# Kernel optimization log

Measured on AMD Instinct MI355X. Metric: run time of the kernel, lower is better.

The kernel has to match this reference:

```python
import jax, jax.numpy as jnp
import numpy as np

B, T, D = 32, 512, 1024
P, E, K = 512, 256, 14
NH, L, FF, TOPK = 4, 2, 2048, 7
FOLD_DIV = 2
EPS = 1e-5


def _ln(x, g, b):
    m = x.mean(-1, keepdims=True)
    v = ((x - m) ** 2).mean(-1, keepdims=True)
    return (x - m) * jax.lax.rsqrt(v + EPS) * g + b


def _bn(x, g, b, m, v):  # eval-mode BatchNorm1d with running stats
    return (x - m) * jax.lax.rsqrt(v + EPS) * g + b


def _attn(q, k, v, nh):
    Bq, Tq, Eq = q.shape
    Tk = k.shape[1]
    hd = Eq // nh
    qh = q.reshape(Bq, Tq, nh, hd).transpose(0, 2, 1, 3)
    kh = k.reshape(Bq, Tk, nh, hd).transpose(0, 2, 1, 3)
    vh = v.reshape(Bq, Tk, nh, hd).transpose(0, 2, 1, 3)
    s = jnp.einsum('bhqd,bhkd->bhqk', qh, kh) / jnp.sqrt(jnp.float32(hd))
    a = jax.nn.softmax(s, axis=-1)
    o = jnp.einsum('bhqk,bhkd->bhqd', a, vh)
    return o.transpose(0, 2, 1, 3).reshape(Bq, Tq, Eq)


def setup_inputs() -> dict:
    key = jax.random.key(0)
    ks = iter(jax.random.split(key, 64))

    def rn(shape, s=0.02):
        return jax.random.normal(next(ks), shape, jnp.float32) * s

    return dict(
        x=jax.random.normal(next(ks), (B, T, D), jnp.float32),
        pred_w=rn((D,)), pred_b=jnp.zeros(()),
        t_wqkv=rn((L, D, 3 * D)), t_bqkv=jnp.zeros((L, 3 * D)),
        t_wo=rn((L, D, D)), t_bo=jnp.zeros((L, D)),
        t_ln1g=jnp.ones((L, D)), t_ln1b=jnp.zeros((L, D)),
        t_w1=rn((L, D, FF)), t_b1=jnp.zeros((L, FF)),
        t_w2=rn((L, FF, D)), t_b2=jnp.zeros((L, D)),
        t_ln2g=jnp.ones((L, D)), t_ln2b=jnp.zeros((L, D)),
        sb_w=rn((D, P)), sb_b=jnp.zeros((P,)),
        bn1_g=jnp.ones((P,)), bn1_b=jnp.zeros((P,)), bn1_m=jnp.zeros((P,)), bn1_v=jnp.ones((P,)),
        dt_w=rn((P,)), dt_b=jnp.zeros(()),
        cc_w1=rn((P, 256)), cc_b1=jnp.zeros((256,)),
        bn2_g=jnp.ones((256,)), bn2_b=jnp.zeros((256,)), bn2_m=jnp.zeros((256,)), bn2_v=jnp.ones((256,)),
        cc_w2=rn((256, K)), cc_b2=jnp.zeros((K,)),
        ce=rn((K, E), 1.0),
        kp_w=rn((P, E)), kp_b=jnp.zeros((E,)),
        ca_wqkv=rn((E, 3 * E)), ca_bqkv=jnp.zeros((3 * E,)),
        ca_wo=rn((E, E)), ca_bo=jnp.zeros((E,)),
        fp_w=rn((E, D)), fp_b=jnp.zeros((D,)),
        df_w=rn((P,)), df_b=jnp.zeros(()),
    )


def reference(x, pred_w, pred_b, t_wqkv, t_bqkv, t_wo, t_bo, t_ln1g, t_ln1b, t_w1, t_b1,
              t_w2, t_b2, t_ln2g, t_ln2b, sb_w, sb_b, bn1_g, bn1_b, bn1_m, bn1_v,
              dt_w, dt_b, cc_w1, cc_b1, bn2_g, bn2_b, bn2_m, bn2_v, cc_w2, cc_b2,
              ce, kp_w, kp_b, ca_wqkv, ca_bqkv, ca_wo, ca_bo, fp_w, fp_b, df_w, df_b):
    # --- GlobalAdaptiveTSM: per-token adaptive channel shift, fully vectorized ---
    ratio = jax.nn.sigmoid(jnp.einsum('btd,d->bt', x, pred_w) + pred_b)  # ShiftPredictor
    fold = D // FOLD_DIV
    sn = (ratio * fold).astype(jnp.int32)[..., None]                     # [B,T,1]
    z = jnp.zeros_like(x[:, :1])
    x_prev = jnp.concatenate([z, x[:, :-1]], axis=1)   # t=0 region stays zero
    x_next = jnp.concatenate([x[:, 1:], z], axis=1)    # t=T-1 region stays zero
    c = jnp.arange(D)
    h = jnp.where(c < sn, x_prev, jnp.where(c < 2 * sn, x_next, x))
    # --- TemporalTransformer: 2 post-norm encoder layers (eval mode) ---
    for l in range(L):
        qkv = h @ t_wqkv[l] + t_bqkv[l]
        q, k, v = jnp.split(qkv, 3, axis=-1)
        a = _attn(q, k, v, NH) @ t_wo[l] + t_bo[l]
        h = _ln(h + a, t_ln1g[l], t_ln1b[l])
        f = jax.nn.relu(h @ t_w1[l] + t_b1[l]) @ t_w2[l] + t_b2[l]
        h = _ln(h + f, t_ln2g[l], t_ln2b[l])

    def backbone(zz):
        return jax.nn.relu(_bn(zz @ sb_w + sb_b, bn1_g, bn1_b, bn1_m, bn1_v))

    shared = backbone(h)                                      # [B,T,P]
    top_scores = jnp.einsum('btp,p->bt', shared, dt_w) + dt_b
    _, idx = jax.lax.top_k(top_scores, TOPK)
    agg = jnp.take_along_axis(shared, idx[..., None], axis=1).mean(1)  # [B,P]
    c1 = jax.nn.relu(_bn(agg @ cc_w1 + cc_b1, bn2_g, bn2_b, bn2_m, bn2_v))
    logits = c1 @ cc_w2 + cc_b2                               # [B,K]
    cat_emb = jax.nn.softmax(logits, axis=-1) @ ce            # [B,E]
    proj = shared @ kp_w + kp_b                               # [B,T,E]
    q = cat_emb[:, None, :] @ ca_wqkv[:, :E] + ca_bqkv[:E]
    k = proj @ ca_wqkv[:, E:2 * E] + ca_bqkv[E:2 * E]
    v = proj @ ca_wqkv[:, 2 * E:] + ca_bqkv[2 * E:]
    ctx = _attn(q, k, v, NH) @ ca_wo + ca_bo                  # [B,1,E] broadcasts over T
    final = proj + ctx
    fin_proj = backbone(final @ fp_w + fp_b)
    seg = jnp.einsum('btp,p->bt', fin_proj, df_w) + df_b
    return seg, logits
```

## Files before the change

### kernel.cpp

```cpp
#include <hip/hip_runtime.h>
#include <math.h>

#define Bz 32
#define Tz 512
#define Dz 1024
#define Pz 512
#define Ez 256
#define KC 14
#define NHz 4
#define Lz 2
#define FFz 2048
#define TOPKz 7
#define EPSz 1e-5f
#define BT (Bz*Tz)

typedef unsigned short ushort_t;
typedef __attribute__((ext_vector_type(8))) short short8;
typedef __attribute__((ext_vector_type(4))) float f32x4;

__device__ __forceinline__ ushort_t f2bf(float f) {
    union { float f; unsigned int u; } x; x.f = f;
    unsigned int r = x.u + 0x7fffu + ((x.u >> 16) & 1u);
    return (ushort_t)(r >> 16);
}
__device__ __forceinline__ float bf2f(ushort_t h) {
    union { unsigned int u; float f; } x; x.u = ((unsigned int)h) << 16; return x.f;
}

__global__ __launch_bounds__(256) void mgemm_k(
    const ushort_t* __restrict__ A, int lda,
    const ushort_t* __restrict__ Wt,
    const float* __restrict__ bias,
    float* __restrict__ Cf, ushort_t* __restrict__ Ch, int ldc,
    int Kd, int epi,
    const float* __restrict__ bng, const float* __restrict__ bnb,
    const float* __restrict__ bnm, const float* __restrict__ bnv)
{
    __shared__ __align__(16) ushort_t As[128 * 32];
    __shared__ __align__(16) ushort_t Bs[128 * 32];
    const int tid = threadIdx.x;
    const int lane = tid & 63, wid = tid >> 6;
    const int row0 = blockIdx.y * 128, col0 = blockIdx.x * 128;
    const int wrow = (wid >> 1) * 64, wcol = (wid & 1) * 64;
    const int srow = (lane >> 2);
    const int skoff = (lane & 3) * 8;

    f32x4 acc[4][4];
    const f32x4 zr = {0.f, 0.f, 0.f, 0.f};
    #pragma unroll
    for (int m = 0; m < 4; m++)
        #pragma unroll
        for (int n = 0; n < 4; n++) acc[m][n] = zr;

    for (int k0 = 0; k0 < Kd; k0 += 32) {
        #pragma unroll
        for (int j = 0; j < 2; j++) {
            const int r = wid * 32 + j * 16;
            const ushort_t* ga = A + (size_t)(row0 + r + srow) * lda + k0 + skoff;
            __builtin_amdgcn_global_load_lds(
                (const __attribute__((address_space(1))) unsigned int*)ga,
                (__attribute__((address_space(3))) unsigned int*)(As + r * 32), 16, 0, 0);
            const ushort_t* gb = Wt + (size_t)(col0 + r + srow) * Kd + k0 + skoff;
            __builtin_amdgcn_global_load_lds(
                (const __attribute__((address_space(1))) unsigned int*)gb,
                (__attribute__((address_space(3))) unsigned int*)(Bs + r * 32), 16, 0, 0);
        }
        __syncthreads();
        short8 af[4], bf[4];
        #pragma unroll
        for (int m = 0; m < 4; m++)
            af[m] = *(const short8*)(As + (wrow + m * 16 + (lane & 15)) * 32 + (lane >> 4) * 8);
        #pragma unroll
        for (int n = 0; n < 4; n++)
            bf[n] = *(const short8*)(Bs + (wcol + n * 16 + (lane & 15)) * 32 + (lane >> 4) * 8);
        #pragma unroll
        for (int m = 0; m < 4; m++)
            #pragma unroll
            for (int n = 0; n < 4; n++)
                acc[m][n] = __builtin_amdgcn_mfma_f32_16x16x32_bf16(af[m], bf[n], acc[m][n], 0, 0, 0);
        __syncthreads();
    }

    #pragma unroll
    for (int n = 0; n < 4; n++) {
        const int ccol = col0 + wcol + n * 16 + (lane & 15);
        const float bb = bias[ccol];
        float bsc = 1.f, bsh = 0.f;
        if (epi == 2) {
            bsc = rsqrtf(bnv[ccol] + EPSz) * bng[ccol];
            bsh = bnb[ccol] - bnm[ccol] * bsc;
        }
        #pragma unroll
        for (int m = 0; m < 4; m++) {
            #pragma unroll
            for (int r = 0; r < 4; r++) {
                const int crow = row0 + wrow + m * 16 + (lane >> 4) * 4 + r;
                float y = acc[m][n][r] + bb;
                if (epi == 2) y = y * bsc + bsh;
                if (epi >= 1) y = fmaxf(y, 0.f);
                if (Cf) Cf[(size_t)crow * ldc + ccol] = y;
                if (Ch) Ch[(size_t)crow * ldc + ccol] = f2bf(y);
            }
        }
    }
}

__global__ __launch_bounds__(256) void bgemm_k(
    const ushort_t* __restrict__ A0, int lda, size_t Abz, int Ahz,
    const ushort_t* __restrict__ W0, int ldw, size_t Wbz, int Whz,
    float* __restrict__ Cf0, ushort_t* __restrict__ Ch0, int ldc, size_t Cbz, int Chz, int Kd)
{
    const int z = blockIdx.z, bl = z >> 2, hh = z & 3;
    const ushort_t* A = A0 + (size_t)bl * Abz + (size_t)hh * Ahz;
    const ushort_t* W = W0 + (size_t)bl * Wbz + (size_t)hh * Whz;

    __shared__ __align__(16) ushort_t As[128 * 32];
    __shared__ __align__(16) ushort_t Bs[128 * 32];
    const int tid = threadIdx.x;
    const int lane = tid & 63, wid = tid >> 6;
    const int row0 = blockIdx.y * 128, col0 = blockIdx.x * 128;
    const int wrow = (wid >> 1) * 64, wcol = (wid & 1) * 64;
    const int srow = (lane >> 2);
    const int skoff = (lane & 3) * 8;

    f32x4 acc[4][4];
    const f32x4 zr = {0.f, 0.f, 0.f, 0.f};
    #pragma unroll
    for (int m = 0; m < 4; m++)
        #pragma unroll
        for (int n = 0; n < 4; n++) acc[m][n] = zr;

    for (int k0 = 0; k0 < Kd; k0 += 32) {
        #pragma unroll
        for (int j = 0; j < 2; j++) {
            const int r = wid * 32 + j * 16;
            const ushort_t* ga = A + (size_t)(row0 + r + srow) * lda + k0 + skoff;
            __builtin_amdgcn_global_load_lds(
                (const __attribute__((address_space(1))) unsigned int*)ga,
                (__attribute__((address_space(3))) unsigned int*)(As + r * 32), 16, 0, 0);
            const ushort_t* gb = W + (size_t)(col0 + r + srow) * ldw + k0 + skoff;
            __builtin_amdgcn_global_load_lds(
                (const __attribute__((address_space(1))) unsigned int*)gb,
                (__attribute__((address_space(3))) unsigned int*)(Bs + r * 32), 16, 0, 0);
        }
        __syncthreads();
        short8 af[4], bf[4];
        #pragma unroll
        for (int m = 0; m < 4; m++)
            af[m] = *(const short8*)(As + (wrow + m * 16 + (lane & 15)) * 32 + (lane >> 4) * 8);
        #pragma unroll
        for (int n = 0; n < 4; n++)
            bf[n] = *(const short8*)(Bs + (wcol + n * 16 + (lane & 15)) * 32 + (lane >> 4) * 8);
        #pragma unroll
        for (int m = 0; m < 4; m++)
            #pragma unroll
            for (int n = 0; n < 4; n++)
                acc[m][n] = __builtin_amdgcn_mfma_f32_16x16x32_bf16(af[m], bf[n], acc[m][n], 0, 0, 0);
        __syncthreads();
    }

    #pragma unroll
    for (int n = 0; n < 4; n++) {
        const int ccol = col0 + wcol + n * 16 + (lane & 15);
        #pragma unroll
        for (int m = 0; m < 4; m++) {
            #pragma unroll
            for (int r = 0; r < 4; r++) {
                const int crow = row0 + wrow + m * 16 + (lane >> 4) * 4 + r;
                const float y = acc[m][n][r];
                if (Cf0) (Cf0 + (size_t)bl * Cbz + (size_t)hh * Chz)[(size_t)crow * ldc + ccol] = y;
                if (Ch0) (Ch0 + (size_t)bl * Cbz + (size_t)hh * Chz)[(size_t)crow * ldc + ccol] = f2bf(y);
            }
        }
    }
}

__global__ __launch_bounds__(256) void qkvt_k(
    const ushort_t* __restrict__ qkvb, ushort_t* __restrict__ Sb, ushort_t* __restrict__ Vt)
{
    __shared__ __align__(16) ushort_t smem[2][128 * 32];
    const int bx = blockIdx.x, z = blockIdx.y;
    const int bl = z >> 2, hh = z & 3;
    const int tid = threadIdx.x;

    if (bx < 16) {
        const ushort_t* A = qkvb + (size_t)bl * 512 * 3072 + hh * 256;
        const ushort_t* W = qkvb + (size_t)bl * 512 * 3072 + 1024 + hh * 256;
        ushort_t* C = Sb + (size_t)z * 512 * 512;
        ushort_t* As = smem[0];
        ushort_t* Bs = smem[1];
        const int lane = tid & 63, wid = tid >> 6;
        const int row0 = (bx >> 2) * 128, col0 = (bx & 3) * 128;
        const int wrow = (wid >> 1) * 64, wcol = (wid & 1) * 64;
        const int srow = (lane >> 2);
        const int skoff = (lane & 3) * 8;

        f32x4 acc[4][4];
        const f32x4 zr = {0.f, 0.f, 0.f, 0.f};
        #pragma unroll
        for (int m = 0; m < 4; m++)
            #pragma unroll
            for (int n = 0; n < 4; n++) acc[m][n] = zr;

        for (int k0 = 0; k0 < 256; k0 += 32) {
            #pragma unroll
            for (int j = 0; j < 2; j++) {
                const int r = wid * 32 + j * 16;
                const ushort_t* ga = A + (size_t)(row0 + r + srow) * 3072 + k0 + skoff;
                __builtin_amdgcn_global_load_lds(
                    (const __attribute__((address_space(1))) unsigned int*)ga,
                    (__attribute__((address_space(3))) unsigned int*)(As + r * 32), 16, 0, 0);
                const ushort_t* gb = W + (size_t)(col0 + r + srow) * 3072 + k0 + skoff;
                __builtin_amdgcn_global_load_lds(
                    (const __attribute__((address_space(1))) unsigned int*)gb,
                    (__attribute__((address_space(3))) unsigned int*)(Bs + r * 32), 16, 0, 0);
            }
            __syncthreads();
            short8 af[4], bf[4];
            #pragma unroll
            for (int m = 0; m < 4; m++)
                af[m] = *(const short8*)(As + (wrow + m * 16 + (lane & 15)) * 32 + (lane >> 4) * 8);
            #pragma unroll
            for (int n = 0; n < 4; n++)
                bf[n] = *(const short8*)(Bs + (wcol + n * 16 + (lane & 15)) * 32 + (lane >> 4) * 8);
            #pragma unroll
            for (int m = 0; m < 4; m++)
                #pragma unroll
                for (int n = 0; n < 4; n++)
                    acc[m][n] = __builtin_amdgcn_mfma_f32_16x16x32_bf16(af[m], bf[n], acc[m][n], 0, 0, 0);
            __syncthreads();
        }

        #pragma unroll
        for (int n = 0; n < 4; n++) {
            const int ccol = col0 + wcol + n * 16 + (lane & 15);
            #pragma unroll
            for (int m = 0; m < 4; m++) {
                #pragma unroll
                for (int r = 0; r < 4; r++) {
                    const int crow = row0 + wrow + m * 16 + (lane >> 4) * 4 + r;
                    C[(size_t)crow * 512 + ccol] = f2bf(acc[m][n][r]);
                }
            }
        }
    } else {
        const int local = bx - 16;
        const int gx = (local & 7) * 32;
        const int gy = (local >> 3) * 32;
        const ushort_t* src = qkvb + (size_t)bl * 512 * 3072 + 2048 + hh * 256;
        ushort_t* dst = Vt + (size_t)z * 256 * 512;
        ushort_t (*t)[33] = (ushort_t(*)[33])smem;
        const int tx = tid & 31, ty = tid >> 5;
        #pragma unroll
        for (int i = 0; i < 4; i++) {
            const int row = ty + i * 8;
            t[row][tx] = src[(size_t)(gy + row) * 3072 + gx + tx];
        }
        __syncthreads();
        #pragma unroll
        for (int i = 0; i < 4; i++) {
            const int nr = ty + i * 8;
            dst[(size_t)(gx + nr) * 512 + gy + tx] = t[tx][nr];
        }
    }
}

__global__ __launch_bounds__(256) void softmax_k(ushort_t* __restrict__ SP)
{
    const int row = blockIdx.x * 4 + (threadIdx.x >> 6);
    const int lane = threadIdx.x & 63;
    ushort_t* rp = SP + (size_t)row * 512 + lane * 8;
    union { ushort_t h[8]; uint4 u; } in;
    in.u = *(const uint4*)rp;
    float v[8];
    #pragma unroll
    for (int i = 0; i < 8; i++) v[i] = bf2f(in.h[i]) * 0.0625f;
    float m = v[0];
    #pragma unroll
    for (int i = 1; i < 8; i++) m = fmaxf(m, v[i]);
    #pragma unroll
    for (int off = 32; off > 0; off >>= 1) m = fmaxf(m, __shfl_xor(m, off));
    float s = 0.f;
    #pragma unroll
    for (int i = 0; i < 8; i++) { v[i] = expf(v[i] - m); s += v[i]; }
    #pragma unroll
    for (int off = 32; off > 0; off >>= 1) s += __shfl_xor(s, off);
    const float inv = 1.f / s;
    union { ushort_t h[8]; uint4 u; } pk;
    #pragma unroll
    for (int i = 0; i < 8; i++) pk.h[i] = f2bf(v[i] * inv);
    *(uint4*)rp = pk.u;
}

struct WtJobs {
    const float* src[13];
    ushort_t*    dst[13];
    int ld[13];
    int Kd[13];
    int nx[13];
    int base[14];
};

__global__ __launch_bounds__(256) void wtall_k(WtJobs J)
{
    const int bid = blockIdx.x;
    int j = 0;
    #pragma unroll
    for (int i = 0; i < 12; i++) if (bid >= J.base[i + 1]) j = i + 1;
    const int local = bid - J.base[j];
    const int bx = local % J.nx[j], by = local / J.nx[j];
    const float* src = J.src[j];
    ushort_t* dst = J.dst[j];
    const int ld = J.ld[j], Kd = J.Kd[j];

    __shared__ float t[32][33];
    const int tx = threadIdx.x & 31, ty = threadIdx.x >> 5;
    const int gx = bx * 32;
    const int gy = by * 32;
    #pragma unroll
    for (int i = 0; i < 4; i++) {
        const int row = ty + i * 8;
        t[row][tx] = src[(size_t)(gy + row) * ld + gx + tx];
    }
    __syncthreads();
    #pragma unroll
    for (int i = 0; i < 4; i++) {
        const int nr = ty + i * 8;
        dst[(size_t)(gx + nr) * Kd + gy + tx] = f2bf(t[tx][nr]);
    }
}

__global__ __launch_bounds__(256) void predshift_k(
    const float* __restrict__ x, const float* __restrict__ pred_w,
    const float* __restrict__ pred_b, ushort_t* __restrict__ hb)
{
    const int row = blockIdx.x, tid = threadIdx.x;
    const size_t base = (size_t)row * Dz;
    float s = 0.f;
    #pragma unroll
    for (int i = 0; i < 4; i++) {
        int c = tid + i * 256;
        s += x[base + c] * pred_w[c];
    }
    __shared__ float red[256];
    __shared__ int sns;
    red[tid] = s; __syncthreads();
    for (int off = 128; off > 0; off >>= 1) {
        if (tid < off) red[tid] += red[tid + off];
        __syncthreads();
    }
    if (tid == 0) {
        float sg = 1.f / (1.f + expf(-(red[0] + pred_b[0])));
        sns = (int)(sg * (float)(Dz / 2));
    }
    __syncthreads();
    const int sn = sns;
    const int t = row & (Tz - 1);
    #pragma unroll
    for (int i = 0; i < 4; i++) {
        const int c = tid + i * 256;
        const size_t idx = base + c;
        float v;
        if (c < sn)          v = (t > 0)      ? x[idx - Dz] : 0.f;
        else if (c < 2 * sn) v = (t < Tz - 1) ? x[idx + Dz] : 0.f;
        else                 v = x[idx];
        hb[idx] = f2bf(v);
    }
}

__global__ __launch_bounds__(256) void addlnb_k(
    ushort_t* __restrict__ hb, const ushort_t* __restrict__ r,
    const float* __restrict__ g, const float* __restrict__ b)
{
    const int row = blockIdx.x, tid = threadIdx.x;
    const size_t base = (size_t)row * Dz;
    float x[4]; float s = 0.f, sq = 0.f;
    #pragma unroll
    for (int i = 0; i < 4; i++) {
        const int c = tid + i * 256;
        x[i] = bf2f(hb[base + c]) + bf2f(r[base + c]);
        s += x[i]; sq += x[i] * x[i];
    }
    __shared__ float rs[256], rq[256];
    rs[tid] = s; rq[tid] = sq; __syncthreads();
    for (int off = 128; off > 0; off >>= 1) {
        if (tid < off) { rs[tid] += rs[tid + off]; rq[tid] += rq[tid + off]; }
        __syncthreads();
    }
    float mean = rs[0] * (1.f / Dz);
    float var = rq[0] * (1.f / Dz) - mean * mean;
    float inv = rsqrtf(var + EPSz);
    #pragma unroll
    for (int i = 0; i < 4; i++) {
        int c = tid + i * 256;
        float y = (x[i] - mean) * inv * g[c] + b[c];
        hb[base + c] = f2bf(y);
    }
}

__global__ __launch_bounds__(256) void rowdot_k(
    const float* __restrict__ in, const float* __restrict__ w,
    const float* __restrict__ bptr, float* __restrict__ outf)
{
    const int row = blockIdx.x, tid = threadIdx.x;
    const float* r = in + (size_t)row * Pz;
    float s = 0.f;
    #pragma unroll
    for (int c = tid; c < Pz; c += 256) s += r[c] * w[c];
    __shared__ float red[256];
    red[tid] = s; __syncthreads();
    for (int off = 128; off > 0; off >>= 1) {
        if (tid < off) red[tid] += red[tid + off];
        __syncthreads();
    }
    if (tid == 0) outf[row] = red[0] + bptr[0];
}

__global__ __launch_bounds__(256) void tailcls_k(
    const float* __restrict__ scores, const float* __restrict__ shared_,
    const float* __restrict__ cc_w1, const float* __restrict__ cc_b1,
    const float* __restrict__ g2, const float* __restrict__ b2,
    const float* __restrict__ m2, const float* __restrict__ v2,
    const float* __restrict__ cc_w2, const float* __restrict__ cc_b2,
    const float* __restrict__ ce,
    const float* __restrict__ ca_wqkv, const float* __restrict__ ca_bqkv,
    float* __restrict__ logits_out, float* __restrict__ qx)
{
    const int b = blockIdx.x, tid = threadIdx.x;
    __shared__ float sv[Tz];
    __shared__ float rv[256]; __shared__ int ri[256];
    __shared__ int tki[TOPKz];
    __shared__ float ag[Pz], c1s[256], sm[16], cemb[256];

    sv[tid] = scores[b * Tz + tid];
    sv[tid + 256] = scores[b * Tz + tid + 256];
    __syncthreads();

    for (int it = 0; it < TOPKz; it++) {
        float v0 = sv[tid]; int i0 = tid;
        float v1 = sv[tid + 256];
        if (v1 > v0) { v0 = v1; i0 = tid + 256; }
        rv[tid] = v0; ri[tid] = i0; __syncthreads();
        for (int off = 128; off > 0; off >>= 1) {
            if (tid < off) {
                if (rv[tid + off] > rv[tid] ||
                    (rv[tid + off] == rv[tid] && ri[tid + off] < ri[tid])) {
                    rv[tid] = rv[tid + off]; ri[tid] = ri[tid + off];
                }
            }
            __syncthreads();
        }
        if (tid == 0) { tki[it] = ri[0]; sv[ri[0]] = -INFINITY; }
        __syncthreads();
    }

    const float* base = shared_ + (size_t)b * Tz * Pz;
    for (int p = tid; p < Pz; p += 256) {
        float s = 0.f;
        #pragma unroll
        for (int j = 0; j < TOPKz; j++) s += base[(size_t)tki[j] * Pz + p];
        ag[p] = s * (1.f / TOPKz);
    }
    __syncthreads();

    float s = 0.f;
    for (int p = 0; p < Pz; p++) s += ag[p] * cc_w1[p * 256 + tid];
    s += cc_b1[tid];
    s = (s - m2[tid]) * rsqrtf(v2[tid] + EPSz) * g2[tid] + b2[tid];
    s = fmaxf(s, 0.f);
    c1s[tid] = s;
    __syncthreads();
    if (tid < KC) {
        float l = 0.f;
        for (int e = 0; e < 256; e++) l += c1s[e] * cc_w2[e * KC + tid];
        l += cc_b2[tid];
        sm[tid] = l;
        logits_out[b * KC + tid] = l;
    }
    __syncthreads();
    if (tid == 0) {
        float mx = sm[0];
        for (int k = 1; k < KC; k++) mx = fmaxf(mx, sm[k]);
        float su = 0.f;
        for (int k = 0; k < KC; k++) { sm[k] = expf(sm[k] - mx); su += sm[k]; }
        float inv = 1.f / su;
        for (int k = 0; k < KC; k++) sm[k] *= inv;
    }
    __syncthreads();
    float cesum = 0.f;
    #pragma unroll
    for (int k = 0; k < KC; k++) cesum += sm[k] * ce[k * 256 + tid];
    cemb[tid] = cesum; __syncthreads();
    float q = 0.f;
    for (int i = 0; i < 256; i++) q += cemb[i] * ca_wqkv[i * 768 + tid];
    qx[b * 256 + tid] = q + ca_bqkv[tid];
}

__global__ __launch_bounds__(256) void xattn_k(
    const float* __restrict__ qx, const float* __restrict__ kv,
    const float* __restrict__ ca_wo, const float* __restrict__ ca_bo,
    float* __restrict__ ctx2)
{
    const int b = blockIdx.x, tid = threadIdx.x;
    __shared__ float q4[256];
    __shared__ float sc[NHz][Tz];
    __shared__ float cx[256];
    q4[tid] = qx[b * 256 + tid];
    __syncthreads();
    for (int si = tid; si < NHz * Tz; si += 256) {
        int hh = si >> 9, t = si & (Tz - 1);
        const float* kr = kv + ((size_t)b * Tz + t) * 512 + hh * 64;
        const float* qr = q4 + hh * 64;
        float s = 0.f;
        #pragma unroll 8
        for (int d = 0; d < 64; d++) s += qr[d] * kr[d];
        sc[hh][t] = s * 0.125f;
    }
    __syncthreads();
    const int hh = tid >> 6, lane = tid & 63;
    float mx = -INFINITY;
    for (int t = lane; t < Tz; t += 64) mx = fmaxf(mx, sc[hh][t]);
    for (int off = 32; off > 0; off >>= 1) mx = fmaxf(mx, __shfl_xor(mx, off));
    float su = 0.f;
    for (int t = lane; t < Tz; t += 64) { float e = expf(sc[hh][t] - mx); sc[hh][t] = e; su += e; }
    for (int off = 32; off > 0; off >>= 1) su += __shfl_xor(su, off);
    float inv = 1.f / su;
    __syncthreads();
    float acc = 0.f;
    for (int t = 0; t < Tz; t++) acc += sc[hh][t] * kv[((size_t)b * Tz + t) * 512 + 256 + tid];
    cx[tid] = acc * inv;
    __syncthreads();
    float s2 = 0.f;
    for (int i = 0; i < 256; i++) s2 += cx[i] * ca_wo[i * 256 + tid];
    ctx2[b * 256 + tid] = s2 + ca_bo[tid];
}

__global__ __launch_bounds__(256) void addctx_k(
    const float* __restrict__ proj, const float* __restrict__ ctx2, ushort_t* __restrict__ fb)
{
    size_t idx = (size_t)blockIdx.x * 256 + threadIdx.x;
    int e = (int)(idx & 255);
    int b = (int)(idx >> 17);
    fb[idx] = f2bf(proj[idx] + ctx2[b * 256 + e]);
}

extern "C" void kernel_launch(void* const* d_in, const int* in_sizes, int n_in,
                              void* d_out, int out_size, void* d_ws, size_t ws_size,
                              hipStream_t stream)
{
    const float* x       = (const float*)d_in[0];
    const float* pred_w  = (const float*)d_in[1];
    const float* pred_b  = (const float*)d_in[2];
    const float* t_wqkv  = (const float*)d_in[3];
    const float* t_bqkv  = (const float*)d_in[4];
    const float* t_wo    = (const float*)d_in[5];
    const float* t_bo    = (const float*)d_in[6];
    const float* t_ln1g  = (const float*)d_in[7];
    const float* t_ln1b  = (const float*)d_in[8];
    const float* t_w1    = (const float*)d_in[9];
    const float* t_b1    = (const float*)d_in[10];
    const float* t_w2    = (const float*)d_in[11];
    const float* t_b2    = (const float*)d_in[12];
    const float* t_ln2g  = (const float*)d_in[13];
    const float* t_ln2b  = (const float*)d_in[14];
    const float* sb_w    = (const float*)d_in[15];
    const float* sb_b    = (const float*)d_in[16];
    const float* bn1_g   = (const float*)d_in[17];
    const float* bn1_b   = (const float*)d_in[18];
    const float* bn1_m   = (const float*)d_in[19];
    const float* bn1_v   = (const float*)d_in[20];
    const float* dt_w    = (const float*)d_in[21];
    const float* dt_b    = (const float*)d_in[22];
    const float* cc_w1   = (const float*)d_in[23];
    const float* cc_b1   = (const float*)d_in[24];
    const float* bn2_g   = (const float*)d_in[25];
    const float* bn2_b   = (const float*)d_in[26];
    const float* bn2_m   = (const float*)d_in[27];
    const float* bn2_v   = (const float*)d_in[28];
    const float* cc_w2   = (const float*)d_in[29];
    const float* cc_b2   = (const float*)d_in[30];
    const float* ce      = (const float*)d_in[31];
    const float* kp_w    = (const float*)d_in[32];
    const float* kp_b    = (const float*)d_in[33];
    const float* ca_wqkv = (const float*)d_in[34];
    const float* ca_bqkv = (const float*)d_in[35];
    const float* ca_wo   = (const float*)d_in[36];
    const float* ca_bo   = (const float*)d_in[37];
    const float* fp_w    = (const float*)d_in[38];
    const float* fp_b    = (const float*)d_in[39];
    const float* df_w    = (const float*)d_in[40];
    const float* df_b    = (const float*)d_in[41];

    float* out = (float*)d_out;

    char* wp = (char*)d_ws;
    auto alloc = [&](size_t bytes) -> char* {
        char* r = wp; wp += (bytes + 255) & ~(size_t)255; return r;
    };
    float* scores  = (float*)alloc(BT * 4);
    float* qxbuf   = (float*)alloc((size_t)Bz * Ez * 4);
    float* ctx2buf = (float*)alloc((size_t)Bz * Ez * 4);

    const size_t WT_TOTAL = 2*(size_t)3072*1024 + 2*(size_t)1024*1024 + 2*(size_t)2048*1024
                          + 2*(size_t)1024*2048 + (size_t)512*1024 + (size_t)256*512
                          + 2*(size_t)256*256 + (size_t)1024*256;
    ushort_t* wtb = (ushort_t*)alloc(WT_TOTAL * 2);
    size_t woff = 0;
    auto nxt = [&](size_t n) -> ushort_t* { ushort_t* r = wtb + woff; woff += n; return r; };
    ushort_t* qkvT[2] = { nxt((size_t)3072*1024), nxt((size_t)3072*1024) };
    ushort_t* woT[2]  = { nxt((size_t)1024*1024), nxt((size_t)1024*1024) };
    ushort_t* w1T[2]  = { nxt((size_t)2048*1024), nxt((size_t)2048*1024) };
    ushort_t* w2T[2]  = { nxt((size_t)1024*2048), nxt((size_t)1024*2048) };
    ushort_t* sbT  = nxt((size_t)512*1024);
    ushort_t* kpT  = nxt((size_t)256*512);
    ushort_t* kvT  = nxt((size_t)512*256);
    ushort_t* fpT  = nxt((size_t)1024*256);

    size_t fixedB = (size_t)(wp - (char*)d_ws);
    int Bc = Bz;
    while (Bc > 1 && fixedB + (size_t)Bc * Tz * 14336 + 1048576 > ws_size) Bc >>= 1;
    const int Rmax = Bc * Tz;
    ushort_t* hb   = (ushort_t*)alloc((size_t)Rmax * 1024 * 2);
    ushort_t* qkvb = (ushort_t*)alloc((size_t)Rmax * 3072 * 2);
    ushort_t* Pb   = (ushort_t*)alloc((size_t)Rmax * 2048 * 2);
    ushort_t* Vt   = (ushort_t*)alloc((size_t)Rmax * 1024 * 2);

    {
        WtJobs J;
        const float* srcs[13] = { t_wqkv, t_wqkv + (size_t)1024*3072, t_wo, t_wo + (size_t)1024*1024,
                                  t_w1, t_w1 + (size_t)1024*2048, t_w2, t_w2 + (size_t)2048*1024,
                                  sb_w, kp_w, ca_wqkv + Ez, ca_wqkv + 2*Ez, fp_w };
        ushort_t* dsts[13] = { qkvT[0], qkvT[1], woT[0], woT[1], w1T[0], w1T[1], w2T[0], w2T[1],
                               sbT, kpT, kvT, kvT + (size_t)256*256, fpT };
        const int lds_[13] = { 3072, 3072, 1024, 1024, 2048, 2048, 1024, 1024, 512, 256, 768, 768, 1024 };
        const int kds_[13] = { 1024, 1024, 1024, 1024, 1024, 1024, 2048, 2048, 1024, 512, 256, 256, 256 };
        const int nxs_[13] = { 96, 96, 32, 32, 64, 64, 32, 32, 16, 8, 8, 8, 32 };
        const int nys_[13] = { 32, 32, 32, 32, 32, 32, 64, 64, 32, 16, 8, 8, 8 };
        int acc = 0;
        for (int i = 0; i < 13; i++) {
            J.src[i] = srcs[i]; J.dst[i] = dsts[i];
            J.ld[i] = lds_[i]; J.Kd[i] = kds_[i]; J.nx[i] = nxs_[i];
            J.base[i] = acc; acc += nxs_[i] * nys_[i];
        }
        J.base[13] = acc;
        wtall_k<<<acc, 256, 0, stream>>>(J);
    }

    for (int b0 = 0; b0 < Bz; b0 += Bc) {
        const int R = Bc * Tz;
        const float* xc = x + (size_t)b0 * Tz * Dz;

        auto MG = [&](const ushort_t* Ain, int lda, const ushort_t* Wt_, const float* bias,
                      float* Cf, ushort_t* Ch, int ldc, int N, int Kd, int epi,
                      const float* g = nullptr, const float* bb = nullptr,
                      const float* m = nullptr, const float* v = nullptr) {
            mgemm_k<<<dim3(N/128, R/128), 256, 0, stream>>>(
                Ain, lda, Wt_, bias, Cf, Ch, ldc, Kd, epi, g, bb, m, v);
        };

        predshift_k<<<R, 256, 0, stream>>>(xc, pred_w, pred_b, hb);

        for (int l = 0; l < Lz; l++) {
            MG(hb, 1024, qkvT[l], t_bqkv + (size_t)l*3072, nullptr, qkvb, 3072, 3072, 1024, 0);
            qkvt_k<<<dim3(144, Bc * 4), 256, 0, stream>>>(qkvb, Pb, Vt);
            softmax_k<<<R, 256, 0, stream>>>(Pb);
            bgemm_k<<<dim3(2, 4, Bc * 4), 256, 0, stream>>>(
                Pb, 512, (size_t)4 * 512 * 512, 512 * 512,
                Vt, 512, (size_t)4 * 256 * 512, 256 * 512,
                nullptr, qkvb, 3072, (size_t)512 * 3072, 256, 512);
            MG(qkvb, 3072, woT[l], t_bo + (size_t)l*1024, nullptr, Pb, 1024, 1024, 1024, 0);
            addlnb_k<<<R, 256, 0, stream>>>(hb, Pb,
                                            t_ln1g + (size_t)l*Dz, t_ln1b + (size_t)l*Dz);
            MG(hb, 1024, w1T[l], t_b1 + (size_t)l*FFz, nullptr, qkvb, 2048, 2048, 1024, 1);
            MG(qkvb, 2048, w2T[l], t_b2 + (size_t)l*Dz, nullptr, Pb, 1024, 1024, 2048, 0);
            addlnb_k<<<R, 256, 0, stream>>>(hb, Pb,
                                            t_ln2g + (size_t)l*Dz, t_ln2b + (size_t)l*Dz);
        }

        float*    shared  = (float*)Vt;
        float*    proj    = (float*)hb;
        float*    kvb     = (float*)(qkvb + (size_t)R * 1024);
        float*    fin     = (float*)(Pb + (size_t)R * 1024);
        ushort_t* sharedb = Pb;
        ushort_t* projb   = Pb + (size_t)R * 512;
        ushort_t* fb      = Pb + (size_t)R * 768;
        ushort_t* fpb     = qkvb;

        MG(hb, 1024, sbT, sb_b, shared, sharedb, 512, 512, 1024, 2, bn1_g, bn1_b, bn1_m, bn1_v);
        rowdot_k<<<R, 256, 0, stream>>>(shared, dt_w, dt_b, scores + (size_t)b0 * Tz);
        tailcls_k<<<Bc, 256, 0, stream>>>(scores + (size_t)b0 * Tz, shared, cc_w1, cc_b1,
                                          bn2_g, bn2_b, bn2_m, bn2_v, cc_w2, cc_b2,
                                          ce, ca_wqkv, ca_bqkv,
                                          out + BT + (size_t)b0 * KC, qxbuf);
        MG(sharedb, 512, kpT, kp_b, proj, projb, 256, 256, 512, 0);
        MG(projb, 256, kvT, ca_bqkv + Ez, kvb, nullptr, 512, 512, 256, 0);
        xattn_k<<<Bc, 256, 0, stream>>>(qxbuf, kvb, ca_wo, ca_bo, ctx2buf);
        addctx_k<<<(R * Ez) / 256, 256, 0, stream>>>(proj, ctx2buf, fb);
        MG(fb, 256, fpT, fp_b, nullptr, fpb, 1024, 1024, 256, 0);
        MG(fpb, 1024, sbT, sb_b, fin, nullptr, 512, 512, 1024, 2, bn1_g, bn1_b, bn1_m, bn1_v);
        rowdot_k<<<R, 256, 0, stream>>>(fin, df_w, df_b, out + (size_t)b0 * Tz);
    }
}
```

Before: 1.757 ms.

## Fuse attention QK^T, softmax and PV into one kernel with LDS-resident probabilities

Measured after the change: 1.520 ms. -13.5%, faster.

```diff
diff --git a/kernel.cpp b/kernel.cpp
--- a/kernel.cpp
+++ b/kernel.cpp
@@ -27,6 +27,10 @@
     union { unsigned int u; float f; } x; x.u = ((unsigned int)h) << 16; return x.f;
 }
 
+#define GLDS(gp, lp) __builtin_amdgcn_global_load_lds( \
+    (const __attribute__((address_space(1))) unsigned int*)(gp), \
+    (__attribute__((address_space(3))) unsigned int*)(lp), 16, 0, 0)
+
 __global__ __launch_bounds__(256) void mgemm_k(
     const ushort_t* __restrict__ A, int lda,
     const ushort_t* __restrict__ Wt,
@@ -56,14 +60,8 @@
         #pragma unroll
         for (int j = 0; j < 2; j++) {
             const int r = wid * 32 + j * 16;
-            const ushort_t* ga = A + (size_t)(row0 + r + srow) * lda + k0 + skoff;
-            __builtin_amdgcn_global_load_lds(
-                (const __attribute__((address_space(1))) unsigned int*)ga,
-                (__attribute__((address_space(3))) unsigned int*)(As + r * 32), 16, 0, 0);
-            const ushort_t* gb = Wt + (size_t)(col0 + r + srow) * Kd + k0 + skoff;
-            __builtin_amdgcn_global_load_lds(
-                (const __attribute__((address_space(1))) unsigned int*)gb,
-                (__attribute__((address_space(3))) unsigned int*)(Bs + r * 32), 16, 0, 0);
+            GLDS(A + (size_t)(row0 + r + srow) * lda + k0 + skoff, As + r * 32);
+            GLDS(Wt + (size_t)(col0 + r + srow) * Kd + k0 + skoff, Bs + r * 32);
         }
         __syncthreads();
         short8 af[4], bf[4];
@@ -105,191 +103,189 @@
     }
 }
 
-__global__ __launch_bounds__(256) void bgemm_k(
-    const ushort_t* __restrict__ A0, int lda, size_t Abz, int Ahz,
-    const ushort_t* __restrict__ W0, int ldw, size_t Wbz, int Whz,
-    float* __restrict__ Cf0, ushort_t* __restrict__ Ch0, int ldc, size_t Cbz, int Chz, int Kd)
+__global__ __launch_bounds__(1024) void flash_k(
+    ushort_t* __restrict__ qkvb, const ushort_t* __restrict__ Vt)
+{
+    __shared__ __align__(16) ushort_t Plds[128 * 512];
+    __shared__ __align__(16) ushort_t Bs2[256 * 32];
+    __shared__ float red[128][4];
+    ushort_t* As = Plds;
+    ushort_t* Bs = Plds + 128 * 32;
+
+    const int z = blockIdx.y, bl = z >> 2, hh = z & 3;
+    const int row0 = blockIdx.x * 128;
+    ushort_t* Qs = qkvb + (size_t)bl * 512 * 3072 + hh * 256;
+    const ushort_t* Ks = qkvb + (size_t)bl * 512 * 3072 + 1024 + hh * 256;
+    const ushort_t* V = Vt + (size_t)z * 256 * 512;
+    const int tid = threadIdx.x, lane = tid & 63, w = tid >> 6;
+    const int wr = w >> 2, wc = w & 3;
+
+    f32x4 acc[2][8];
+    const f32x4 zr = {0.f, 0.f, 0.f, 0.f};
+    #pragma unroll
+    for (int m = 0; m < 2; m++)
+        #pragma unroll
+        for (int n = 0; n < 8; n++) acc[m][n] = zr;
+
+    for (int d0 = 0; d0 < 256; d0 += 32) {
+        if (w < 8) {
+            const int rbu = w * 16;
+            const int row = rbu + (lane >> 2);
+            GLDS(Qs + (size_t)(row0 + row) * 3072 + d0 + (lane & 3) * 8, As + rbu * 32);
+        } else {
+            #pragma unroll
+            for (int i = 0; i < 4; i++) {
+                const int rbu = (w - 8) * 64 + i * 16;
+                const int row = rbu + (lane >> 2);
+                GLDS(Ks + (size_t)row * 3072 + d0 + (lane & 3) * 8, Bs + rbu * 32);
+            }
+        }
+        __syncthreads();
+        short8 af[2];
+        #pragma unroll
+        for (int m = 0; m < 2; m++)
+            af[m] = *(const short8*)(As + (wr * 32 + m * 16 + (lane & 15)) * 32 + (lane >> 4) * 8);
+        #pragma unroll
+        for (int n = 0; n < 8; n++) {
+            const short8 bfv = *(const short8*)(Bs + (wc * 128 + n * 16 + (lane & 15)) * 32 + (lane >> 4) * 8);
+            #pragma unroll
+            for (int m = 0; m < 2; m++)
+                acc[m][n] = __builtin_amdgcn_mfma_f32_16x16x32_bf16(af[m], bfv, acc[m][n], 0, 0, 0);
+        }
+        __syncthreads();
+    }
+
+    #pragma unroll
+    for (int m = 0; m < 2; m++)
+        #pragma unroll
+        for (int n = 0; n < 8; n++) acc[m][n] *= 0.0625f;
+
+    float rmx[2][4], rinv[2][4];
+    #pragma unroll
+    for (int m = 0; m < 2; m++)
+        #pragma unroll
+        for (int r = 0; r < 4; r++) {
+            float mx = acc[m][0][r];
+            #pragma unroll
+            for (int n = 1; n < 8; n++) mx = fmaxf(mx, acc[m][n][r]);
+            mx = fmaxf(mx, __shfl_xor(mx, 1));
+            mx = fmaxf(mx, __shfl_xor(mx, 2));
+            mx = fmaxf(mx, __shfl_xor(mx, 4));
+            mx = fmaxf(mx, __shfl_xor(mx, 8));
+            if ((lane & 15) == 0) red[wr * 32 + m * 16 + (lane >> 4) * 4 + r][wc] = mx;
+        }
+    __syncthreads();
+    #pragma unroll
+    for (int m = 0; m < 2; m++)
+        #pragma unroll
+        for (int r = 0; r < 4; r++) {
+            const int rw = wr * 32 + m * 16 + (lane >> 4) * 4 + r;
+            rmx[m][r] = fmaxf(fmaxf(red[rw][0], red[rw][1]), fmaxf(red[rw][2], red[rw][3]));
+        }
+    __syncthreads();
+    #pragma unroll
+    for (int m = 0; m < 2; m++)
+        #pragma unroll
+        for (int r = 0; r < 4; r++) {
+            float s = 0.f;
+            #pragma unroll
+            for (int n = 0; n < 8; n++) {
+                const float e = expf(acc[m][n][r] - rmx[m][r]);
+                acc[m][n][r] = e; s += e;
+            }
+            s += __shfl_xor(s, 1); s += __shfl_xor(s, 2);
+            s += __shfl_xor(s, 4); s += __shfl_xor(s, 8);
+            if ((lane & 15) == 0) red[wr * 32 + m * 16 + (lane >> 4) * 4 + r][wc] = s;
+        }
+    __syncthreads();
+    #pragma unroll
+    for (int m = 0; m < 2; m++)
+        #pragma unroll
+        for (int r = 0; r < 4; r++) {
+            const int rw = wr * 32 + m * 16 + (lane >> 4) * 4 + r;
+            rinv[m][r] = 1.f / (red[rw][0] + red[rw][1] + red[rw][2] + red[rw][3]);
+        }
+    __syncthreads();
+
+    char* Pc = (char*)Plds;
+    #pragma unroll
+    for (int m = 0; m < 2; m++)
+        #pragma unroll
+        for (int r = 0; r < 4; r++) {
+            const int rw = wr * 32 + m * 16 + (lane >> 4) * 4 + r;
+            const int rx = (rw & 7) << 4;
+            #pragma unroll
+            for (int n = 0; n < 8; n++) {
+                const int col = wc * 128 + n * 16 + (lane & 15);
+                *(ushort_t*)(Pc + (((rw * 512 + col) * 2) ^ rx)) = f2bf(acc[m][n][r] * rinv[m][r]);
+            }
+        }
+    __syncthreads();
+
+    f32x4 acc2[2][4];
+    #pragma unroll
+    for (int m = 0; m < 2; m++)
+        #pragma unroll
+        for (int n = 0; n < 4; n++) acc2[m][n] = zr;
+
+    for (int k0 = 0; k0 < 512; k0 += 32) {
+        {
+            const int rbu = w * 16;
+            const int row = rbu + (lane >> 2);
+            GLDS(V + (size_t)row * 512 + k0 + (lane & 3) * 8, Bs2 + rbu * 32);
+        }
+        __syncthreads();
+        short8 af2[2];
+        #pragma unroll
+        for (int m = 0; m < 2; m++) {
+            const int rw = wr * 32 + m * 16 + (lane & 15);
+            const int rx = (rw & 7) << 4;
+            af2[m] = *(const short8*)(Pc + (((rw * 512 + k0 + (lane >> 4) * 8) * 2) ^ rx));
+        }
+        #pragma unroll
+        for (int n = 0; n < 4; n++) {
+            const short8 bfv = *(const short8*)(Bs2 + (wc * 64 + n * 16 + (lane & 15)) * 32 + (lane >> 4) * 8);
+            #pragma unroll
+            for (int m = 0; m < 2; m++)
+                acc2[m][n] = __builtin_amdgcn_mfma_f32_16x16x32_bf16(af2[m], bfv, acc2[m][n], 0, 0, 0);
+        }
+        __syncthreads();
+    }
+
+    #pragma unroll
+    for (int n = 0; n < 4; n++) {
+        const int ccol = wc * 64 + n * 16 + (lane & 15);
+        #pragma unroll
+        for (int m = 0; m < 2; m++)
+            #pragma unroll
+            for (int r = 0; r < 4; r++) {
+                const int crow = row0 + wr * 32 + m * 16 + (lane >> 4) * 4 + r;
+                Qs[(size_t)crow * 3072 + ccol] = f2bf(acc2[m][n][r]);
+            }
+    }
+}
+
+__global__ __launch_bounds__(256) void vtb_k(
+    const ushort_t* __restrict__ qkvb, ushort_t* __restrict__ Vt)
 {
     const int z = blockIdx.z, bl = z >> 2, hh = z & 3;
-    const ushort_t* A = A0 + (size_t)bl * Abz + (size_t)hh * Ahz;
-    const ushort_t* W = W0 + (size_t)bl * Wbz + (size_t)hh * Whz;
-
-    __shared__ __align__(16) ushort_t As[128 * 32];
-    __shared__ __align__(16) ushort_t Bs[128 * 32];
-    const int tid = threadIdx.x;
-    const int lane = tid & 63, wid = tid >> 6;
-    const int row0 = blockIdx.y * 128, col0 = blockIdx.x * 128;
-    const int wrow = (wid >> 1) * 64, wcol = (wid & 1) * 64;
-    const int srow = (lane >> 2);
-    const int skoff = (lane & 3) * 8;
-
-    f32x4 acc[4][4];
-    const f32x4 zr = {0.f, 0.f, 0.f, 0.f};
-    #pragma unroll
-    for (int m = 0; m < 4; m++)
-        #pragma unroll
-        for (int n = 0; n < 4; n++) acc[m][n] = zr;
-
-    for (int k0 = 0; k0 < Kd; k0 += 32) {
-        #pragma unroll
-        for (int j = 0; j < 2; j++) {
-            const int r = wid * 32 + j * 16;
-            const ushort_t* ga = A + (size_t)(row0 + r + srow) * lda + k0 + skoff;
-            __builtin_amdgcn_global_load_lds(
-                (const __attribute__((address_space(1))) unsigned int*)ga,
-                (__attribute__((address_space(3))) unsigned int*)(As + r * 32), 16, 0, 0);
-            const ushort_t* gb = W + (size_t)(col0 + r + srow) * ldw + k0 + skoff;
-            __builtin_amdgcn_global_load_lds(
-                (const __attribute__((address_space(1))) unsigned int*)gb,
-                (__attribute__((address_space(3))) unsigned int*)(Bs + r * 32), 16, 0, 0);
-        }
-        __syncthreads();
-        short8 af[4], bf[4];
-        #pragma unroll
-        for (int m = 0; m < 4; m++)
-            af[m] = *(const short8*)(As + (wrow + m * 16 + (lane & 15)) * 32 + (lane >> 4) * 8);
-        #pragma unroll
-        for (int n = 0; n < 4; n++)
-            bf[n] = *(const short8*)(Bs + (wcol + n * 16 + (lane & 15)) * 32 + (lane >> 4) * 8);
-        #pragma unroll
-        for (int m = 0; m < 4; m++)
-            #pragma unroll
-            for (int n = 0; n < 4; n++)
-                acc[m][n] = __builtin_amdgcn_mfma_f32_16x16x32_bf16(af[m], bf[n], acc[m][n], 0, 0, 0);
-        __syncthreads();
-    }
-
-    #pragma unroll
-    for (int n = 0; n < 4; n++) {
-        const int ccol = col0 + wcol + n * 16 + (lane & 15);
-        #pragma unroll
-        for (int m = 0; m < 4; m++) {
-            #pragma unroll
-            for (int r = 0; r < 4; r++) {
-                const int crow = row0 + wrow + m * 16 + (lane >> 4) * 4 + r;
-                const float y = acc[m][n][r];
-                if (Cf0) (Cf0 + (size_t)bl * Cbz + (size_t)hh * Chz)[(size_t)crow * ldc + ccol] = y;
-                if (Ch0) (Ch0 + (size_t)bl * Cbz + (size_t)hh * Chz)[(size_t)crow * ldc + ccol] = f2bf(y);
-            }
-        }
-    }
-}
-
-__global__ __launch_bounds__(256) void qkvt_k(
-    const ushort_t* __restrict__ qkvb, ushort_t* __restrict__ Sb, ushort_t* __restrict__ Vt)
-{
-    __shared__ __align__(16) ushort_t smem[2][128 * 32];
-    const int bx = blockIdx.x, z = blockIdx.y;
-    const int bl = z >> 2, hh = z & 3;
-    const int tid = threadIdx.x;
-
-    if (bx < 16) {
-        const ushort_t* A = qkvb + (size_t)bl * 512 * 3072 + hh * 256;
-        const ushort_t* W = qkvb + (size_t)bl * 512 * 3072 + 1024 + hh * 256;
-        ushort_t* C = Sb + (size_t)z * 512 * 512;
-        ushort_t* As = smem[0];
-        ushort_t* Bs = smem[1];
-        const int lane = tid & 63, wid = tid >> 6;
-        const int row0 = (bx >> 2) * 128, col0 = (bx & 3) * 128;
-        const int wrow = (wid >> 1) * 64, wcol = (wid & 1) * 64;
-        const int srow = (lane >> 2);
-        const int skoff = (lane & 3) * 8;
-
-        f32x4 acc[4][4];
-        const f32x4 zr = {0.f, 0.f, 0.f, 0.f};
-        #pragma unroll
-        for (int m = 0; m < 4; m++)
-            #pragma unroll
-            for (int n = 0; n < 4; n++) acc[m][n] = zr;
-
-        for (int k0 = 0; k0 < 256; k0 += 32) {
-            #pragma unroll
-            for (int j = 0; j < 2; j++) {
-                const int r = wid * 32 + j * 16;
-                const ushort_t* ga = A + (size_t)(row0 + r + srow) * 3072 + k0 + skoff;
-                __builtin_amdgcn_global_load_lds(
-                    (const __attribute__((address_space(1))) unsigned int*)ga,
-                    (__attribute__((address_space(3))) unsigned int*)(As + r * 32), 16, 0, 0);
-                const ushort_t* gb = W + (size_t)(col0 + r + srow) * 3072 + k0 + skoff;
-                __builtin_amdgcn_global_load_lds(
-                    (const __attribute__((address_space(1))) unsigned int*)gb,
-                    (__attribute__((address_space(3))) unsigned int*)(Bs + r * 32), 16, 0, 0);
-            }
-            __syncthreads();
-            short8 af[4], bf[4];
-            #pragma unroll
-            for (int m = 0; m < 4; m++)
-                af[m] = *(const short8*)(As + (wrow + m * 16 + (lane & 15)) * 32 + (lane >> 4) * 8);
-            #pragma unroll
-            for (int n = 0; n < 4; n++)
-                bf[n] = *(const short8*)(Bs + (wcol + n * 16 + (lane & 15)) * 32 + (lane >> 4) * 8);
-            #pragma unroll
-            for (int m = 0; m < 4; m++)
-                #pragma unroll
-                for (int n = 0; n < 4; n++)
-                    acc[m][n] = __builtin_amdgcn_mfma_f32_16x16x32_bf16(af[m], bf[n], acc[m][n], 0, 0, 0);
-            __syncthreads();
-        }
-
-        #pragma unroll
-        for (int n = 0; n < 4; n++) {
-            const int ccol = col0 + wcol + n * 16 + (lane & 15);
-            #pragma unroll
-            for (int m = 0; m < 4; m++) {
-                #pragma unroll
-                for (int r = 0; r < 4; r++) {
-                    const int crow = row0 + wrow + m * 16 + (lane >> 4) * 4 + r;
-                    C[(size_t)crow * 512 + ccol] = f2bf(acc[m][n][r]);
-                }
-            }
-        }
-    } else {
-        const int local = bx - 16;
-        const int gx = (local & 7) * 32;
-        const int gy = (local >> 3) * 32;
-        const ushort_t* src = qkvb + (size_t)bl * 512 * 3072 + 2048 + hh * 256;
-        ushort_t* dst = Vt + (size_t)z * 256 * 512;
-        ushort_t (*t)[33] = (ushort_t(*)[33])smem;
-        const int tx = tid & 31, ty = tid >> 5;
-        #pragma unroll
-        for (int i = 0; i < 4; i++) {
-            const int row = ty + i * 8;
-            t[row][tx] = src[(size_t)(gy + row) * 3072 + gx + tx];
-        }
-        __syncthreads();
-        #pragma unroll
-        for (int i = 0; i < 4; i++) {
-            const int nr = ty + i * 8;
-            dst[(size_t)(gx + nr) * 512 + gy + tx] = t[tx][nr];
-        }
-    }
-}
-
-__global__ __launch_bounds__(256) void softmax_k(ushort_t* __restrict__ SP)
-{
-    const int row = blockIdx.x * 4 + (threadIdx.x >> 6);
-    const int lane = threadIdx.x & 63;
-    ushort_t* rp = SP + (size_t)row * 512 + lane * 8;
-    union { ushort_t h[8]; uint4 u; } in;
-    in.u = *(const uint4*)rp;
-    float v[8];
-    #pragma unroll
-    for (int i = 0; i < 8; i++) v[i] = bf2f(in.h[i]) * 0.0625f;
-    float m = v[0];
-    #pragma unroll
-    for (int i = 1; i < 8; i++) m = fmaxf(m, v[i]);
-    #pragma unroll
-    for (int off = 32; off > 0; off >>= 1) m = fmaxf(m, __shfl_xor(m, off));
-    float s = 0.f;
-    #pragma unroll
-    for (int i = 0; i < 8; i++) { v[i] = expf(v[i] - m); s += v[i]; }
-    #pragma unroll
-    for (int off = 32; off > 0; off >>= 1) s += __shfl_xor(s, off);
-    const float inv = 1.f / s;
-    union { ushort_t h[8]; uint4 u; } pk;
-    #pragma unroll
-    for (int i = 0; i < 8; i++) pk.h[i] = f2bf(v[i] * inv);
-    *(uint4*)rp = pk.u;
+    const ushort_t* src = qkvb + (size_t)bl * 512 * 3072 + 2048 + hh * 256;
+    ushort_t* dst = Vt + (size_t)z * 256 * 512;
+    __shared__ ushort_t t[32][33];
+    const int tx = threadIdx.x & 31, ty = threadIdx.x >> 5;
+    const int gx = blockIdx.x * 32;
+    const int gy = blockIdx.y * 32;
+    #pragma unroll
+    for (int i = 0; i < 4; i++) {
+        const int row = ty + i * 8;
+        t[row][tx] = src[(size_t)(gy + row) * 3072 + gx + tx];
+    }
+    __syncthreads();
+    #pragma unroll
+    for (int i = 0; i < 4; i++) {
+        const int nr = ty + i * 8;
+        dst[(size_t)(gx + nr) * 512 + gy + tx] = t[tx][nr];
+    }
 }
 
 struct WtJobs {
@@ -464,6 +460,7 @@
     __syncthreads();
 
     float s = 0.f;
+    #pragma unroll 8
     for (int p = 0; p < Pz; p++) s += ag[p] * cc_w1[p * 256 + tid];
     s += cc_b1[tid];
     s = (s - m2[tid]) * rsqrtf(v2[tid] + EPSz) * g2[tid] + b2[tid];
@@ -472,6 +469,7 @@
     __syncthreads();
     if (tid < KC) {
         float l = 0.f;
+        #pragma unroll 8
         for (int e = 0; e < 256; e++) l += c1s[e] * cc_w2[e * KC + tid];
         l += cc_b2[tid];
         sm[tid] = l;
@@ -492,6 +490,7 @@
     for (int k = 0; k < KC; k++) cesum += sm[k] * ce[k * 256 + tid];
     cemb[tid] = cesum; __syncthreads();
     float q = 0.f;
+    #pragma unroll 8
     for (int i = 0; i < 256; i++) q += cemb[i] * ca_wqkv[i * 768 + tid];
     qx[b * 256 + tid] = q + ca_bqkv[tid];
 }
@@ -527,10 +526,12 @@
     float inv = 1.f / su;
     __syncthreads();
     float acc = 0.f;
+    #pragma unroll 8
     for (int t = 0; t < Tz; t++) acc += sc[hh][t] * kv[((size_t)b * Tz + t) * 512 + 256 + tid];
     cx[tid] = acc * inv;
     __syncthreads();
     float s2 = 0.f;
+    #pragma unroll 8
     for (int i = 0; i < 256; i++) s2 += cx[i] * ca_wo[i * 256 + tid];
     ctx2[b * 256 + tid] = s2 + ca_bo[tid];
 }
@@ -618,11 +619,11 @@
 
     size_t fixedB = (size_t)(wp - (char*)d_ws);
     int Bc = Bz;
-    while (Bc > 1 && fixedB + (size_t)Bc * Tz * 14336 + 1048576 > ws_size) Bc >>= 1;
+    while (Bc > 1 && fixedB + (size_t)Bc * Tz * 12288 + 1048576 > ws_size) Bc >>= 1;
     const int Rmax = Bc * Tz;
     ushort_t* hb   = (ushort_t*)alloc((size_t)Rmax * 1024 * 2);
     ushort_t* qkvb = (ushort_t*)alloc((size_t)Rmax * 3072 * 2);
-    ushort_t* Pb   = (ushort_t*)alloc((size_t)Rmax * 2048 * 2);
+    ushort_t* Pb   = (ushort_t*)alloc((size_t)Rmax * 1024 * 2);
     ushort_t* Vt   = (ushort_t*)alloc((size_t)Rmax * 1024 * 2);
 
     {
@@ -662,12 +663,8 @@
 
         for (int l = 0; l < Lz; l++) {
             MG(hb, 1024, qkvT[l], t_bqkv + (size_t)l*3072, nullptr, qkvb, 3072, 3072, 1024, 0);
-            qkvt_k<<<dim3(144, Bc * 4), 256, 0, stream>>>(qkvb, Pb, Vt);
-            softmax_k<<<R, 256, 0, stream>>>(Pb);
-            bgemm_k<<<dim3(2, 4, Bc * 4), 256, 0, stream>>>(
-                Pb, 512, (size_t)4 * 512 * 512, 512 * 512,
-                Vt, 512, (size_t)4 * 256 * 512, 256 * 512,
-                nullptr, qkvb, 3072, (size_t)512 * 3072, 256, 512);
+            vtb_k<<<dim3(8, 16, Bc * 4), 256, 0, stream>>>(qkvb, Vt);
+            flash_k<<<dim3(4, Bc * 4), 1024, 0, stream>>>(qkvb, Vt);
             MG(qkvb, 3072, woT[l], t_bo + (size_t)l*1024, nullptr, Pb, 1024, 1024, 1024, 0);
             addlnb_k<<<R, 256, 0, stream>>>(hb, Pb,
                                             t_ln1g + (size_t)l*Dz, t_ln1b + (size_t)l*Dz);
@@ -680,7 +677,7 @@
         float*    shared  = (float*)Vt;
         float*    proj    = (float*)hb;
         float*    kvb     = (float*)(qkvb + (size_t)R * 1024);
-        float*    fin     = (float*)(Pb + (size_t)R * 1024);
+        float*    fin     = (float*)(qkvb + (size_t)R * 2048);
         ushort_t* sharedb = Pb;
         ushort_t* projb   = Pb + (size_t)R * 512;
         ushort_t* fb      = Pb + (size_t)R * 768;
```
